# Optimization experiments

Hardware: AMD Instinct MI355X
Metric: run time of the kernel (lower is better)

Reference implementation:

```python
import jax, jax.numpy as jnp
import numpy as np

B, S, D, H = 2, 2048, 2048, 16
NOPE, ROPE, V, C = 128, 64, 128, 512
EPS = 1e-6


def _rope(x, cos, sin):
    # x: [b,s,h,d] with d even; consecutive pairs form complex numbers (torch view_as_complex)
    b, s, h, d = x.shape
    x2 = x.reshape(b, s, h, d // 2, 2)
    xr, xi = x2[..., 0], x2[..., 1]
    c = cos[None, :, None, :]
    sn = sin[None, :, None, :]
    yr = xr * c - xi * sn
    yi = xr * sn + xi * c
    return jnp.stack([yr, yi], axis=-1).reshape(b, s, h, d)


def _rmsnorm(x, w):
    return x * jax.lax.rsqrt(jnp.mean(x * x, axis=-1, keepdims=True) + EPS) * w


def setup_inputs() -> dict:
    key = jax.random.key(0)
    ks = jax.random.split(key, 6)
    x = jax.random.normal(ks[0], (B, S, D), jnp.float32)
    # xavier-ish scaled weights (torch layout: [out, in])
    wq = jax.random.normal(ks[1], (H * (NOPE + ROPE), D), jnp.float32) * (D ** -0.5)
    wkv_a = jax.random.normal(ks[2], (C + ROPE, D), jnp.float32) * (D ** -0.5)
    kv_norm_w = jnp.ones((C,), jnp.float32)
    wkv_b = jax.random.normal(ks[3], (H * (NOPE + V), C), jnp.float32) * (C ** -0.5)
    wo = jax.random.normal(ks[4], (D, H * V), jnp.float32) * ((H * V) ** -0.5)
    # rope freqs (theta=10000), cos/sin of shape [S, ROPE//2]
    inv = 1.0 / (10000.0 ** (np.arange(0, ROPE, 2, dtype=np.float32) / ROPE))
    ang = np.outer(np.arange(S, dtype=np.float32), inv)
    cos = jnp.asarray(np.cos(ang), jnp.float32)
    sin = jnp.asarray(np.sin(ang), jnp.float32)
    # causal additive mask [S, S]
    idx = jnp.arange(S)
    mask = jnp.where(idx[None, :] <= idx[:, None], 0.0, -1e9).astype(jnp.float32)
    return dict(x=x, cos=cos, sin=sin, mask=mask, wq=wq, wkv_a=wkv_a,
                kv_norm_w=kv_norm_w, wkv_b=wkv_b, wo=wo)


def reference(x, cos, sin, mask, wq, wkv_a, kv_norm_w, wkv_b, wo):
    scale = (NOPE + ROPE) ** -0.5
    # Q projection -> [B,S,H,NOPE+ROPE]
    q = (x @ wq.T).reshape(B, S, H, NOPE + ROPE)
    q_nope, q_pe = q[..., :NOPE], q[..., NOPE:]
    q_pe = _rope(q_pe, cos, sin)
    # low-rank KV latent + shared rope key
    kvr = x @ wkv_a.T                      # [B,S,C+ROPE]
    kv, k_pe = kvr[..., :C], kvr[..., C:]
    k_pe = _rope(k_pe[:, :, None, :], cos, sin)[:, :, 0, :]   # [B,S,ROPE]
    # absorb-mode: fold wkv_b's nope part into q
    wb = wkv_b.reshape(H, NOPE + V, C)
    q_abs = jnp.einsum('bshd,hdc->bshc', q_nope, wb[:, :NOPE])
    kvn = _rmsnorm(kv, kv_norm_w)          # latent cache [B,S,C]
    scores = (jnp.einsum('bshc,btc->bsht', q_abs, kvn)
              + jnp.einsum('bshr,btr->bsht', q_pe, k_pe)) * scale
    scores = scores + mask[None, :, None, :]
    p = jax.nn.softmax(scores.astype(jnp.float32), axis=-1).astype(x.dtype)
    o = jnp.einsum('bsht,btc->bshc', p, kvn)
    o = jnp.einsum('bshc,hdc->bshd', o, wb[:, NOPE:])   # un-absorb value proj
    return o.reshape(B, S, H * V) @ wo.T
```

## Files before the change

kernel.cpp:

```cpp
#include <hip/hip_runtime.h>
#include <hip/hip_bf16.h>

#define B_ 2
#define S_ 2048
#define H_ 16

typedef unsigned short ushort_t;
typedef unsigned int uint_t;
typedef __attribute__((ext_vector_type(8))) short bf16x8;
typedef __attribute__((ext_vector_type(4))) float f32x4;

__device__ __forceinline__ ushort_t f2bf(float f) {
    uint_t u = __float_as_uint(f);
    return (ushort_t)((u + 0x7fffu + ((u >> 16) & 1u)) >> 16);
}
__device__ __forceinline__ float bf2f(ushort_t v) {
    return __uint_as_float(((uint_t)v) << 16);
}

__device__ __forceinline__ void gl_lds16(const ushort_t* g, ushort_t* l) {
    __builtin_amdgcn_global_load_lds(
        (const __attribute__((address_space(1))) unsigned int*)(unsigned long long)g,
        (__attribute__((address_space(3))) unsigned int*)(unsigned int)(unsigned long long)l,
        16, 0, 0);
}

__global__ __launch_bounds__(256) void cast_bf16(const float* __restrict__ src,
                                                 ushort_t* __restrict__ dst, int n)
{
    int i = (blockIdx.x * 256 + threadIdx.x) * 4;
    if (i < n) {
        float4 v = *(const float4*)(src + i);
        ushort_t pk[4] = { f2bf(v.x), f2bf(v.y), f2bf(v.z), f2bf(v.w) };
        *(uint2*)(dst + i) = *(const uint2*)pk;
    }
}

__global__ __launch_bounds__(256) void cast2_bf16(const float* __restrict__ src,
                                                  ushort_t* __restrict__ hi,
                                                  ushort_t* __restrict__ lo, int n)
{
    int i = (blockIdx.x * 256 + threadIdx.x) * 4;
    if (i < n) {
        float4 v = *(const float4*)(src + i);
        float vv[4] = { v.x, v.y, v.z, v.w };
        ushort_t ph[4], pl[4];
#pragma unroll
        for (int k = 0; k < 4; k++) {
            ph[k] = f2bf(vv[k]);
            pl[k] = f2bf(vv[k] - bf2f(ph[k]));
        }
        *(uint2*)(hi + i) = *(const uint2*)ph;
        *(uint2*)(lo + i) = *(const uint2*)pl;
    }
}

__global__ __launch_bounds__(256, 2) void gemm_bf16(const ushort_t* __restrict__ A,
                                                    const ushort_t* __restrict__ Bm,
                                                    float* __restrict__ Cf,
                                                    ushort_t* __restrict__ Cb,
                                                    int M, int N, int K,
                                                    int ldc, int Nreal, int mode)
{
    __shared__ __align__(16) ushort_t As[2][8192];
    __shared__ __align__(16) ushort_t Bs[2][8192];
    const int tid = threadIdx.x;
    const int wv = tid >> 6, lane = tid & 63, l16 = lane & 15, quad = lane >> 4;
    const int wm = wv >> 1, wn = wv & 1;
    const int m0 = blockIdx.y * 128, n0 = blockIdx.x * 128;
    const int srow = lane >> 3;
    const int sch  = ((lane & 7) ^ srow) * 8;

    f32x4 acc[16];
#pragma unroll
    for (int i = 0; i < 16; i++) acc[i] = (f32x4)(0.f);

#pragma unroll
    for (int p = 0; p < 4; p++) {
        int g = wv + p*4, row = g*8 + srow;
        int rowb = n0 + row; if (rowb > Nreal - 1) rowb = Nreal - 1;
        gl_lds16(A  + (size_t)(m0 + row) * K + sch, &As[0][g*512]);
        gl_lds16(Bm + (size_t)rowb * K + sch,       &Bs[0][g*512]);
    }
    __syncthreads();

    int cur = 0;
    for (int k0 = 0; k0 < K; k0 += 64) {
        if (k0 + 64 < K) {
#pragma unroll
            for (int p = 0; p < 4; p++) {
                int g = wv + p*4, row = g*8 + srow;
                int rowb = n0 + row; if (rowb > Nreal - 1) rowb = Nreal - 1;
                gl_lds16(A  + (size_t)(m0 + row) * K + k0 + 64 + sch, &As[cur^1][g*512]);
                gl_lds16(Bm + (size_t)rowb * K + k0 + 64 + sch,       &Bs[cur^1][g*512]);
            }
        }
#pragma unroll
        for (int ks = 0; ks < 2; ks++) {
            bf16x8 af[4], bfr[4];
#pragma unroll
            for (int mt = 0; mt < 4; mt++) {
                int row = wm*64 + mt*16 + l16;
                af[mt] = *(const bf16x8*)(&As[cur][row*64 + (((ks*4+quad) ^ (l16&7))*8)]);
            }
#pragma unroll
            for (int nt = 0; nt < 4; nt++) {
                int row = wn*64 + nt*16 + l16;
                bfr[nt] = *(const bf16x8*)(&Bs[cur][row*64 + (((ks*4+quad) ^ (l16&7))*8)]);
            }
#pragma unroll
            for (int mt = 0; mt < 4; mt++)
#pragma unroll
                for (int nt = 0; nt < 4; nt++)
                    acc[mt*4+nt] = __builtin_amdgcn_mfma_f32_16x16x32_bf16(af[mt], bfr[nt], acc[mt*4+nt], 0, 0, 0);
        }
        __syncthreads();
        cur ^= 1;
    }
#pragma unroll
    for (int mt = 0; mt < 4; mt++)
#pragma unroll
        for (int nt = 0; nt < 4; nt++) {
            int cc = n0 + wn*64 + nt*16 + l16;
            if (cc < Nreal) {
#pragma unroll
                for (int r = 0; r < 4; r++) {
                    size_t rr = m0 + wm*64 + mt*16 + quad*4 + r;
                    float v = acc[mt*4+nt][r];
                    if (mode == 1)      Cb[rr*ldc + cc] = f2bf(v);
                    else if (mode == 2) Cf[rr*ldc + cc] += v;
                    else                Cf[rr*ldc + cc] = v;
                }
            }
        }
}

__global__ __launch_bounds__(256, 2) void gemm_kv3(const ushort_t* __restrict__ Ahg,
                                                   const ushort_t* __restrict__ Alg,
                                                   const ushort_t* __restrict__ Bhg,
                                                   const ushort_t* __restrict__ Blg,
                                                   float* __restrict__ Cf)
{
    __shared__ __align__(16) ushort_t Ah[8192];
    __shared__ __align__(16) ushort_t Al[8192];
    __shared__ __align__(16) ushort_t Bh[8192];
    __shared__ __align__(16) ushort_t Bl[8192];
    const int tid = threadIdx.x;
    const int wv = tid >> 6, lane = tid & 63, l16 = lane & 15, quad = lane >> 4;
    const int wm = wv >> 1, wn = wv & 1;
    const int m0 = blockIdx.y * 128, n0 = blockIdx.x * 128;
    const int srow = lane >> 3;
    const int sch  = ((lane & 7) ^ srow) * 8;
    const int K = 2048;

    f32x4 acc[16];
#pragma unroll
    for (int i = 0; i < 16; i++) acc[i] = (f32x4)(0.f);

    for (int k0 = 0; k0 < K; k0 += 64) {
#pragma unroll
        for (int p = 0; p < 4; p++) {
            int g = wv + p*4, row = g*8 + srow;
            int rowb = n0 + row; if (rowb > 575) rowb = 575;
            gl_lds16(Ahg + (size_t)(m0 + row)*K + k0 + sch, Ah + g*512);
            gl_lds16(Alg + (size_t)(m0 + row)*K + k0 + sch, Al + g*512);
            gl_lds16(Bhg + (size_t)rowb*K + k0 + sch,       Bh + g*512);
            gl_lds16(Blg + (size_t)rowb*K + k0 + sch,       Bl + g*512);
        }
        __syncthreads();
#pragma unroll
        for (int ks = 0; ks < 2; ks++) {
            bf16x8 ah[4], al[4], bh[4], bl[4];
#pragma unroll
            for (int mt = 0; mt < 4; mt++) {
                int off = (wm*64 + mt*16 + l16)*64 + (((ks*4+quad) ^ (l16&7))*8);
                ah[mt] = *(const bf16x8*)(Ah + off);
                al[mt] = *(const bf16x8*)(Al + off);
            }
#pragma unroll
            for (int nt = 0; nt < 4; nt++) {
                int off = (wn*64 + nt*16 + l16)*64 + (((ks*4+quad) ^ (l16&7))*8);
                bh[nt] = *(const bf16x8*)(Bh + off);
                bl[nt] = *(const bf16x8*)(Bl + off);
            }
#pragma unroll
            for (int mt = 0; mt < 4; mt++)
#pragma unroll
                for (int nt = 0; nt < 4; nt++) {
                    acc[mt*4+nt] = __builtin_amdgcn_mfma_f32_16x16x32_bf16(ah[mt], bh[nt], acc[mt*4+nt], 0, 0, 0);
                    acc[mt*4+nt] = __builtin_amdgcn_mfma_f32_16x16x32_bf16(al[mt], bh[nt], acc[mt*4+nt], 0, 0, 0);
                    acc[mt*4+nt] = __builtin_amdgcn_mfma_f32_16x16x32_bf16(ah[mt], bl[nt], acc[mt*4+nt], 0, 0, 0);
                }
        }
        __syncthreads();
    }
#pragma unroll
    for (int mt = 0; mt < 4; mt++)
#pragma unroll
        for (int nt = 0; nt < 4; nt++) {
            int cc = n0 + wn*64 + nt*16 + l16;
            if (cc < 576) {
#pragma unroll
                for (int r = 0; r < 4; r++) {
                    size_t rr = m0 + wm*64 + mt*16 + quad*4 + r;
                    Cf[rr*576 + cc] = acc[mt*4+nt][r];
                }
            }
        }
}

__global__ __launch_bounds__(256, 2) void gemm_vp(const ushort_t* __restrict__ kvnb,
                                                  const ushort_t* __restrict__ wbvB,
                                                  ushort_t* __restrict__ vpT)
{
    __shared__ __align__(16) ushort_t As[2][8192];
    __shared__ __align__(16) ushort_t Bs[2][8192];
    const int tid = threadIdx.x;
    const int wv = tid >> 6, lane = tid & 63, l16 = lane & 15, quad = lane >> 4;
    const int wm = wv >> 1, wn = wv & 1;
    const int m0 = blockIdx.x * 128;
    const int h  = blockIdx.y;
    const ushort_t* Bh = wbvB + h*65536;
    const int srow = lane >> 3;
    const int sch  = ((lane & 7) ^ srow) * 8;

    f32x4 acc[16];
#pragma unroll
    for (int i = 0; i < 16; i++) acc[i] = (f32x4)(0.f);

#pragma unroll
    for (int p = 0; p < 4; p++) {
        int g = wv + p*4, row = g*8 + srow;
        gl_lds16(kvnb + (size_t)(m0 + row)*512 + sch, &As[0][g*512]);
        gl_lds16(Bh   + (size_t)row*512 + sch,        &Bs[0][g*512]);
    }
    __syncthreads();

    int cur = 0;
    for (int k0 = 0; k0 < 512; k0 += 64) {
        if (k0 + 64 < 512) {
#pragma unroll
            for (int p = 0; p < 4; p++) {
                int g = wv + p*4, row = g*8 + srow;
                gl_lds16(kvnb + (size_t)(m0 + row)*512 + k0 + 64 + sch, &As[cur^1][g*512]);
                gl_lds16(Bh   + (size_t)row*512 + k0 + 64 + sch,        &Bs[cur^1][g*512]);
            }
        }
#pragma unroll
        for (int ks = 0; ks < 2; ks++) {
            bf16x8 af[4], bfr[4];
#pragma unroll
            for (int mt = 0; mt < 4; mt++) {
                int row = wm*64 + mt*16 + l16;
                af[mt] = *(const bf16x8*)(&As[cur][row*64 + (((ks*4+quad) ^ (l16&7))*8)]);
            }
#pragma unroll
            for (int nt = 0; nt < 4; nt++) {
                int row = wn*64 + nt*16 + l16;
                bfr[nt] = *(const bf16x8*)(&Bs[cur][row*64 + (((ks*4+quad) ^ (l16&7))*8)]);
            }
#pragma unroll
            for (int mt = 0; mt < 4; mt++)
#pragma unroll
                for (int nt = 0; nt < 4; nt++)
                    acc[mt*4+nt] = __builtin_amdgcn_mfma_f32_16x16x32_bf16(af[mt], bfr[nt], acc[mt*4+nt], 0, 0, 0);
        }
        __syncthreads();
        cur ^= 1;
    }
#pragma unroll
    for (int mt = 0; mt < 4; mt++)
#pragma unroll
        for (int nt = 0; nt < 4; nt++) {
            int rr = m0 + wm*64 + mt*16 + quad*4;
            int bb = rr >> 11, t = rr & 2047;
            int cc = wn*64 + nt*16 + l16;
            ushort_t pk[4];
#pragma unroll
            for (int r = 0; r < 4; r++) pk[r] = f2bf(acc[mt*4+nt][r]);
            *(uint2*)(vpT + ((size_t)((bb*16 + h)*128 + cc))*2048 + t) = *(const uint2*)pk;
        }
}

__global__ __launch_bounds__(256, 2) void gemm_kp(const ushort_t* __restrict__ kvnb,
                                                  const ushort_t* __restrict__ wbkN,
                                                  ushort_t* __restrict__ kpb)
{
    __shared__ __align__(16) ushort_t As[2][8192];
    __shared__ __align__(16) ushort_t Bs[2][8192];
    const int tid = threadIdx.x;
    const int wv = tid >> 6, lane = tid & 63, l16 = lane & 15, quad = lane >> 4;
    const int wm = wv >> 1, wn = wv & 1;
    const int m0 = blockIdx.x * 128;
    const int h  = blockIdx.y;
    const ushort_t* Bh = wbkN + h*65536;
    const int srow = lane >> 3;
    const int sch  = ((lane & 7) ^ srow) * 8;
    const float scale = 0.07216878364870323f;

    f32x4 acc[16];
#pragma unroll
    for (int i = 0; i < 16; i++) acc[i] = (f32x4)(0.f);

#pragma unroll
    for (int p = 0; p < 4; p++) {
        int g = wv + p*4, row = g*8 + srow;
        gl_lds16(kvnb + (size_t)(m0 + row)*512 + sch, &As[0][g*512]);
        gl_lds16(Bh   + (size_t)row*512 + sch,        &Bs[0][g*512]);
    }
    __syncthreads();

    int cur = 0;
    for (int k0 = 0; k0 < 512; k0 += 64) {
        if (k0 + 64 < 512) {
#pragma unroll
            for (int p = 0; p < 4; p++) {
                int g = wv + p*4, row = g*8 + srow;
                gl_lds16(kvnb + (size_t)(m0 + row)*512 + k0 + 64 + sch, &As[cur^1][g*512]);
                gl_lds16(Bh   + (size_t)row*512 + k0 + 64 + sch,        &Bs[cur^1][g*512]);
            }
        }
#pragma unroll
        for (int ks = 0; ks < 2; ks++) {
            bf16x8 af[4], bfr[4];
#pragma unroll
            for (int mt = 0; mt < 4; mt++) {
                int row = wm*64 + mt*16 + l16;
                af[mt] = *(const bf16x8*)(&As[cur][row*64 + (((ks*4+quad) ^ (l16&7))*8)]);
            }
#pragma unroll
            for (int nt = 0; nt < 4; nt++) {
                int row = wn*64 + nt*16 + l16;
                bfr[nt] = *(const bf16x8*)(&Bs[cur][row*64 + (((ks*4+quad) ^ (l16&7))*8)]);
            }
#pragma unroll
            for (int mt = 0; mt < 4; mt++)
#pragma unroll
                for (int nt = 0; nt < 4; nt++)
                    acc[mt*4+nt] = __builtin_amdgcn_mfma_f32_16x16x32_bf16(af[mt], bfr[nt], acc[mt*4+nt], 0, 0, 0);
        }
        __syncthreads();
        cur ^= 1;
    }
#pragma unroll
    for (int mt = 0; mt < 4; mt++)
#pragma unroll
        for (int nt = 0; nt < 4; nt++) {
            int cc = wn*64 + nt*16 + l16;
#pragma unroll
            for (int r = 0; r < 4; r++) {
                int rr = m0 + wm*64 + mt*16 + quad*4 + r;
                int bb = rr >> 11, t = rr & 2047;
                kpb[((size_t)((bb*16 + h)*2048 + t))*128 + cc] = f2bf(acc[mt*4+nt][r] * scale);
            }
        }
}

__global__ __launch_bounds__(256) void prep_wb(const float* __restrict__ wkv_b,
                                               ushort_t* __restrict__ wbkN,
                                               ushort_t* __restrict__ wbvB)
{
    int u = blockIdx.x * 256 + threadIdx.x;
    int h = u >> 16, rem = u & 65535;
    wbkN[u] = f2bf(wkv_b[h*131072 + rem]);
    wbvB[u] = f2bf(wkv_b[h*131072 + 65536 + rem]);
}

__global__ __launch_bounds__(256) void kv_norm_rope(const float* __restrict__ kvr,
                                                    const float* __restrict__ w,
                                                    const float* __restrict__ cosT,
                                                    const float* __restrict__ sinT,
                                                    ushort_t* __restrict__ kvnb,
                                                    ushort_t* __restrict__ kpeb)
{
    const int bs   = blockIdx.x * 4 + (threadIdx.x >> 6);
    const int lane = threadIdx.x & 63;
    const int s    = bs & (S_ - 1);
    const float* row = kvr + bs * 576;
    const float scale = 0.07216878364870323f;

    float4 v0 = *(const float4*)(row + lane*8);
    float4 v1 = *(const float4*)(row + lane*8 + 4);
    float ss = v0.x*v0.x + v0.y*v0.y + v0.z*v0.z + v0.w*v0.w
             + v1.x*v1.x + v1.y*v1.y + v1.z*v1.z + v1.w*v1.w;
#pragma unroll
    for (int off = 32; off >= 1; off >>= 1) ss += __shfl_xor(ss, off);
    const float rs = rsqrtf(ss * (1.0f/512.0f) + 1e-6f);

    float4 w0 = *(const float4*)(w + lane*8);
    float4 w1 = *(const float4*)(w + lane*8 + 4);
    float o[8];
    o[0] = v0.x*rs*w0.x; o[1] = v0.y*rs*w0.y; o[2] = v0.z*rs*w0.z; o[3] = v0.w*rs*w0.w;
    o[4] = v1.x*rs*w1.x; o[5] = v1.y*rs*w1.y; o[6] = v1.z*rs*w1.z; o[7] = v1.w*rs*w1.w;

    ushort_t pk[8];
#pragma unroll
    for (int p = 0; p < 8; p++) pk[p] = f2bf(o[p]);
    *(uint4*)(kvnb + (size_t)bs*512 + lane*8) = *(const uint4*)pk;

    if (lane < 32) {
        float xr = row[512 + 2*lane], xi = row[512 + 2*lane + 1];
        float c  = cosT[s*32 + lane], sn = sinT[s*32 + lane];
        ushort_t p2[2] = { f2bf((xr*c - xi*sn)*scale), f2bf((xr*sn + xi*c)*scale) };
        *(uint_t*)(kpeb + (size_t)bs*64 + 2*lane) = *(const uint_t*)p2;
    }
}

__device__ __forceinline__ void stage_tile(const ushort_t* kp_h, const ushort_t* kpe_b,
                                           const ushort_t* vpT_h, ushort_t* ldsb,
                                           int t0, int buf, int w, int l16, int q8e)
{
    ushort_t* Fb = ldsb + buf*6144;
    ushort_t* Vb = ldsb + 12288 + buf*4096;
#pragma unroll
    for (int ii = 0; ii < 3; ii++) {
        int i = w + ii*8;
        if (i < 12) {
            int g2 = (i >= 6) ? 1 : 0;
            int ks = i - g2*6;
            int row = t0 + g2*16 + l16;
            const ushort_t* src = (ks < 4)
                ? (kp_h + (size_t)row*128 + ks*32 + q8e)
                : (kpe_b + (size_t)row*64 + (ks-4)*32 + q8e);
            gl_lds16(src, Fb + i*512);
        } else if (i < 20) {
            int gv = i - 12;
            const ushort_t* src = vpT_h + (size_t)(gv*16 + l16)*2048 + t0 + q8e;
            gl_lds16(src, Vb + gv*512);
        }
    }
}

__global__ __launch_bounds__(512, 2) void attn_mfma(
    const ushort_t* __restrict__ qb,
    const ushort_t* __restrict__ kpb,
    const ushort_t* __restrict__ kpeb,
    const ushort_t* __restrict__ vpT,
    const float* __restrict__ cosT,
    const float* __restrict__ sinT,
    ushort_t* __restrict__ ovb)
{
    const int flat = blockIdx.x + 16*blockIdx.y + 256*blockIdx.z;
    const int b    = flat & 1;
    const int rem  = flat >> 1;
    const int h    = rem & 15;
    const int q0   = (15 - (rem >> 4)) << 7;

    const int tid  = threadIdx.x;
    const int w    = tid >> 6;
    const int lane = tid & 63;
    const int l16  = lane & 15;
    const int quad = lane >> 4;
    const int tl   = quad * 4;
    const int lb   = lane & 48;
    const int q8e  = quad * 8;

    __shared__ __align__(16) ushort_t lds[25600];

    const ushort_t* kp_h  = kpb + (size_t)(b*16 + h)*2048*128;
    const ushort_t* kpe_b = kpeb + (size_t)b*S_*64;
    const ushort_t* vpT_h = vpT + (size_t)(b*16 + h)*128*2048;

    const int r0    = q0 + w*16;
    const int rglob = r0 + l16;

    stage_tile(kp_h, kpe_b, vpT_h, lds, 0, 0, w, l16, q8e);

    const ushort_t* qrow = qb + (size_t)(b*S_ + rglob)*3072 + h*192;
    bf16x8 qf[6];
#pragma unroll
    for (int ks = 0; ks < 4; ks++)
        qf[ks] = *(const bf16x8*)(qrow + ks*32 + q8e);
#pragma unroll
    for (int kk = 0; kk < 2; kk++) {
        int off = kk*32 + q8e;
        uint4 pv4 = *(const uint4*)(qrow + 128 + off);
        const ushort_t* pe = (const ushort_t*)&pv4;
        ushort_t pk[8];
#pragma unroll
        for (int u2 = 0; u2 < 4; u2++) {
            float xr = bf2f(pe[2*u2]), xi = bf2f(pe[2*u2+1]);
            int pi = (off >> 1) + u2;
            float c = cosT[rglob*32 + pi], sn = sinT[rglob*32 + pi];
            pk[2*u2]   = f2bf(xr*c  - xi*sn);
            pk[2*u2+1] = f2bf(xr*sn + xi*c );
        }
        qf[4 + kk] = *(const bf16x8*)pk;
    }
    __syncthreads();

    f32x4 o[8];
#pragma unroll
    for (int n = 0; n < 8; n++) o[n] = (f32x4)(0.f);
    float m_s = -1e30f, l_s = 0.f;

    const int bniter = (q0 >> 5) + 4;
    const int wniter = ((r0 + 15) >> 5) + 1;
    ushort_t* ptw = lds + 20480 + w*640;
    int cur = 0;

#pragma unroll 1
    for (int it = 0; it < bniter; it++) {
        if (it + 1 < bniter)
            stage_tile(kp_h, kpe_b, vpT_h, lds, (it+1)*32, cur ^ 1, w, l16, q8e);

        if (it < wniter) {
            const int t0 = it * 32;
            const ushort_t* Fb = lds + cur*6144;
            const ushort_t* Vb = lds + 12288 + cur*4096;

            __builtin_amdgcn_s_setprio(1);
            f32x4 s0 = (f32x4)(0.f), s1 = (f32x4)(0.f);
#pragma unroll
            for (int ks = 0; ks < 6; ks++) {
                bf16x8 kf0 = *(const bf16x8*)(Fb + ks*512 + lane*8);
                s0 = __builtin_amdgcn_mfma_f32_16x16x32_bf16(kf0, qf[ks], s0, 0, 0, 0);
                bf16x8 kf1 = *(const bf16x8*)(Fb + 3072 + ks*512 + lane*8);
                s1 = __builtin_amdgcn_mfma_f32_16x16x32_bf16(kf1, qf[ks], s1, 0, 0, 0);
            }
            __builtin_amdgcn_s_setprio(0);

            float pv[8];
            float mx = -1e30f;
#pragma unroll
            for (int reg = 0; reg < 4; reg++) {
                pv[reg]   = ((t0 + tl + reg)      <= rglob) ? s0[reg] : -1e30f;
                pv[4+reg] = ((t0 + 16 + tl + reg) <= rglob) ? s1[reg] : -1e30f;
                mx = fmaxf(mx, fmaxf(pv[reg], pv[4+reg]));
            }
            mx = fmaxf(mx, __shfl_xor(mx, 16));
            mx = fmaxf(mx, __shfl_xor(mx, 32));
            if (!__all(mx <= m_s)) {
                float mn = fmaxf(m_s, mx);
                float al = __expf(m_s - mn);
                m_s = mn;
                l_s *= al;
                f32x4 alv;
#pragma unroll
                for (int reg = 0; reg < 4; reg++) alv[reg] = __shfl(al, lb + tl + reg, 64);
#pragma unroll
                for (int n = 0; n < 8; n++) o[n] *= alv;
            }
            float ps = 0.f;
#pragma unroll
            for (int reg = 0; reg < 8; reg++) {
                pv[reg] = (pv[reg] > -1e29f) ? __expf(pv[reg] - m_s) : 0.f;
                ps += pv[reg];
            }
            ps += __shfl_xor(ps, 16);
            ps += __shfl_xor(ps, 32);
            l_s += ps;

            ushort_t pk4[8];
#pragma unroll
            for (int reg = 0; reg < 8; reg++) pk4[reg] = f2bf(pv[reg]);
            *(uint2*)(ptw + l16*40 + tl)      = *(const uint2*)(pk4);
            *(uint2*)(ptw + l16*40 + 16 + tl) = *(const uint2*)(pk4 + 4);
            asm volatile("" ::: "memory");
            bf16x8 ap = *(const bf16x8*)(ptw + l16*40 + q8e);
            asm volatile("" ::: "memory");

            __builtin_amdgcn_s_setprio(1);
#pragma unroll
            for (int n = 0; n < 8; n++) {
                bf16x8 bv = *(const bf16x8*)(Vb + n*512 + lane*8);
                o[n] = __builtin_amdgcn_mfma_f32_16x16x32_bf16(ap, bv, o[n], 0, 0, 0);
            }
            __builtin_amdgcn_s_setprio(0);
        }
        __syncthreads();
        cur ^= 1;
    }

    float linv = 1.f / l_s;
    f32x4 rlv;
#pragma unroll
    for (int reg = 0; reg < 4; reg++) rlv[reg] = __shfl(linv, lb + tl + reg, 64);

    ushort_t* orow = ovb + (size_t)(b*S_ + r0)*2048 + h*128;
#pragma unroll
    for (int n = 0; n < 8; n++)
#pragma unroll
        for (int reg = 0; reg < 4; reg++)
            orow[(size_t)(tl + reg)*2048 + n*16 + l16] = f2bf(o[n][reg] * rlv[reg]);
}

extern "C" void kernel_launch(void* const* d_in, const int* in_sizes, int n_in,
                              void* d_out, int out_size, void* d_ws, size_t ws_size,
                              hipStream_t stream) {
    const float* x     = (const float*)d_in[0];
    const float* cosT  = (const float*)d_in[1];
    const float* sinT  = (const float*)d_in[2];
    const float* wq    = (const float*)d_in[4];
    const float* wkv_a = (const float*)d_in[5];
    const float* kvw   = (const float*)d_in[6];
    const float* wkv_b = (const float*)d_in[7];
    const float* wo    = (const float*)d_in[8];
    float* out = (float*)d_out;

    ushort_t* qb   = (ushort_t*)d_ws;
    ushort_t* xb   = qb   + 12582912;
    ushort_t* wqb  = xb   + 8388608;
    ushort_t* wob  = wqb  + 6291456;
    ushort_t* ovb  = wob  + 4194304;
    ushort_t* kvnb = ovb  + 8388608;
    ushort_t* kpeb = kvnb + 2097152;
    ushort_t* kvnT = kpeb + 262144;
    ushort_t* wbkN = kvnT + 2097152;
    ushort_t* wbvB = wbkN + 1048576;
    float*    kvr  = (float*)(wbvB + 1048576);

    ushort_t* xlo  = ovb;
    ushort_t* wahi = wqb;
    ushort_t* walo = wqb + 1179648;
    ushort_t* vpT  = xb;
    ushort_t* kpb  = wqb;

    dim3 blk(256);
    cast2_bf16<<<dim3(8192), blk, 0, stream>>>(x, xb, xlo, 8388608);
    cast_bf16<<<dim3(6144), blk, 0, stream>>>(wq, wqb, 6291456);
    prep_wb<<<dim3(4096), blk, 0, stream>>>(wkv_b, wbkN, wbvB);
    gemm_bf16<<<dim3(24, 32), blk, 0, stream>>>(xb, wqb, nullptr, qb, 4096, 3072, 2048, 3072, 3072, 1);
    cast2_bf16<<<dim3(1152), blk, 0, stream>>>(wkv_a, wahi, walo, 1179648);
    gemm_kv3<<<dim3(5, 32), blk, 0, stream>>>(xb, xlo, wahi, walo, kvr);
    kv_norm_rope<<<dim3(1024), blk, 0, stream>>>(kvr, kvw, cosT, sinT, kvnb, kpeb);
    gemm_vp<<<dim3(32, 16), blk, 0, stream>>>(kvnb, wbvB, vpT);
    gemm_kp<<<dim3(32, 16), blk, 0, stream>>>(kvnb, wbkN, kpb);
    attn_mfma<<<dim3(16, 16, 2), dim3(512), 0, stream>>>(qb, kpb, kpeb, vpT, cosT, sinT, ovb);
    cast_bf16<<<dim3(4096), blk, 0, stream>>>(wo, wob, 4194304);
    gemm_bf16<<<dim3(16, 32), blk, 0, stream>>>(ovb, wob, out, nullptr, 4096, 2048, 2048, 2048, 2048, 0);
}
```

Before: 478.9 us.

## Fuse K/V projection GEMMs, fold log2e into scale, skip masking on full tiles

Merges the separate key-projection and value-projection GEMMs into one kernel that loads the kvn tile once and accumulates against both weight halves. This removes a launch and a second read of kvn, but drops double-buffering and doubles accumulator registers. The attention scale now includes log2(e) so softmax can use exp2f. Causal masking is skipped for tiles lying fully below the diagonal, and probabilities are packed to bf16 with a hardware packed-convert instruction.

```diff
diff --git a/kernel.cpp b/kernel.cpp
--- a/kernel.cpp
+++ b/kernel.cpp
@@ -209,150 +209,75 @@
         }
 }
 
-__global__ __launch_bounds__(256, 2) void gemm_vp(const ushort_t* __restrict__ kvnb,
+__global__ __launch_bounds__(256, 2) void gemm_vk(const ushort_t* __restrict__ kvnb,
+                                                  const ushort_t* __restrict__ wbkN,
                                                   const ushort_t* __restrict__ wbvB,
+                                                  ushort_t* __restrict__ kpb,
                                                   ushort_t* __restrict__ vpT)
 {
-    __shared__ __align__(16) ushort_t As[2][8192];
-    __shared__ __align__(16) ushort_t Bs[2][8192];
+    __shared__ __align__(16) ushort_t As[8192];
+    __shared__ __align__(16) ushort_t Bk[8192];
+    __shared__ __align__(16) ushort_t Bv[8192];
     const int tid = threadIdx.x;
     const int wv = tid >> 6, lane = tid & 63, l16 = lane & 15, quad = lane >> 4;
     const int wm = wv >> 1, wn = wv & 1;
     const int m0 = blockIdx.x * 128;
     const int h  = blockIdx.y;
-    const ushort_t* Bh = wbvB + h*65536;
+    const ushort_t* Bkh = wbkN + h*65536;
+    const ushort_t* Bvh = wbvB + h*65536;
     const int srow = lane >> 3;
     const int sch  = ((lane & 7) ^ srow) * 8;
-
-    f32x4 acc[16];
-#pragma unroll
-    for (int i = 0; i < 16; i++) acc[i] = (f32x4)(0.f);
-
-#pragma unroll
-    for (int p = 0; p < 4; p++) {
-        int g = wv + p*4, row = g*8 + srow;
-        gl_lds16(kvnb + (size_t)(m0 + row)*512 + sch, &As[0][g*512]);
-        gl_lds16(Bh   + (size_t)row*512 + sch,        &Bs[0][g*512]);
-    }
-    __syncthreads();
-
-    int cur = 0;
+    const float SC2 = 0.10411756512f;
+
+    f32x4 ak[16], av[16];
+#pragma unroll
+    for (int i = 0; i < 16; i++) { ak[i] = (f32x4)(0.f); av[i] = (f32x4)(0.f); }
+
     for (int k0 = 0; k0 < 512; k0 += 64) {
-        if (k0 + 64 < 512) {
-#pragma unroll
-            for (int p = 0; p < 4; p++) {
-                int g = wv + p*4, row = g*8 + srow;
-                gl_lds16(kvnb + (size_t)(m0 + row)*512 + k0 + 64 + sch, &As[cur^1][g*512]);
-                gl_lds16(Bh   + (size_t)row*512 + k0 + 64 + sch,        &Bs[cur^1][g*512]);
-            }
-        }
+#pragma unroll
+        for (int p = 0; p < 4; p++) {
+            int g = wv + p*4, row = g*8 + srow;
+            gl_lds16(kvnb + (size_t)(m0 + row)*512 + k0 + sch, As + g*512);
+            gl_lds16(Bkh  + (size_t)row*512 + k0 + sch,        Bk + g*512);
+            gl_lds16(Bvh  + (size_t)row*512 + k0 + sch,        Bv + g*512);
+        }
+        __syncthreads();
 #pragma unroll
         for (int ks = 0; ks < 2; ks++) {
-            bf16x8 af[4], bfr[4];
-#pragma unroll
-            for (int mt = 0; mt < 4; mt++) {
-                int row = wm*64 + mt*16 + l16;
-                af[mt] = *(const bf16x8*)(&As[cur][row*64 + (((ks*4+quad) ^ (l16&7))*8)]);
-            }
+            bf16x8 af[4], bkf[4], bvf[4];
+#pragma unroll
+            for (int mt = 0; mt < 4; mt++)
+                af[mt] = *(const bf16x8*)(As + (wm*64 + mt*16 + l16)*64 + (((ks*4+quad) ^ (l16&7))*8));
 #pragma unroll
             for (int nt = 0; nt < 4; nt++) {
-                int row = wn*64 + nt*16 + l16;
-                bfr[nt] = *(const bf16x8*)(&Bs[cur][row*64 + (((ks*4+quad) ^ (l16&7))*8)]);
+                int off = (wn*64 + nt*16 + l16)*64 + (((ks*4+quad) ^ (l16&7))*8);
+                bkf[nt] = *(const bf16x8*)(Bk + off);
+                bvf[nt] = *(const bf16x8*)(Bv + off);
             }
 #pragma unroll
             for (int mt = 0; mt < 4; mt++)
 #pragma unroll
-                for (int nt = 0; nt < 4; nt++)
-                    acc[mt*4+nt] = __builtin_amdgcn_mfma_f32_16x16x32_bf16(af[mt], bfr[nt], acc[mt*4+nt], 0, 0, 0);
+                for (int nt = 0; nt < 4; nt++) {
+                    ak[mt*4+nt] = __builtin_amdgcn_mfma_f32_16x16x32_bf16(af[mt], bkf[nt], ak[mt*4+nt], 0, 0, 0);
+                    av[mt*4+nt] = __builtin_amdgcn_mfma_f32_16x16x32_bf16(af[mt], bvf[nt], av[mt*4+nt], 0, 0, 0);
+                }
         }
         __syncthreads();
-        cur ^= 1;
-    }
-#pragma unroll
-    for (int mt = 0; mt < 4; mt++)
-#pragma unroll
-        for (int nt = 0; nt < 4; nt++) {
-            int rr = m0 + wm*64 + mt*16 + quad*4;
-            int bb = rr >> 11, t = rr & 2047;
-            int cc = wn*64 + nt*16 + l16;
-            ushort_t pk[4];
-#pragma unroll
-            for (int r = 0; r < 4; r++) pk[r] = f2bf(acc[mt*4+nt][r]);
-            *(uint2*)(vpT + ((size_t)((bb*16 + h)*128 + cc))*2048 + t) = *(const uint2*)pk;
-        }
-}
-
-__global__ __launch_bounds__(256, 2) void gemm_kp(const ushort_t* __restrict__ kvnb,
-                                                  const ushort_t* __restrict__ wbkN,
-                                                  ushort_t* __restrict__ kpb)
-{
-    __shared__ __align__(16) ushort_t As[2][8192];
-    __shared__ __align__(16) ushort_t Bs[2][8192];
-    const int tid = threadIdx.x;
-    const int wv = tid >> 6, lane = tid & 63, l16 = lane & 15, quad = lane >> 4;
-    const int wm = wv >> 1, wn = wv & 1;
-    const int m0 = blockIdx.x * 128;
-    const int h  = blockIdx.y;
-    const ushort_t* Bh = wbkN + h*65536;
-    const int srow = lane >> 3;
-    const int sch  = ((lane & 7) ^ srow) * 8;
-    const float scale = 0.07216878364870323f;
-
-    f32x4 acc[16];
-#pragma unroll
-    for (int i = 0; i < 16; i++) acc[i] = (f32x4)(0.f);
-
-#pragma unroll
-    for (int p = 0; p < 4; p++) {
-        int g = wv + p*4, row = g*8 + srow;
-        gl_lds16(kvnb + (size_t)(m0 + row)*512 + sch, &As[0][g*512]);
-        gl_lds16(Bh   + (size_t)row*512 + sch,        &Bs[0][g*512]);
-    }
-    __syncthreads();
-
-    int cur = 0;
-    for (int k0 = 0; k0 < 512; k0 += 64) {
-        if (k0 + 64 < 512) {
-#pragma unroll
-            for (int p = 0; p < 4; p++) {
-                int g = wv + p*4, row = g*8 + srow;
-                gl_lds16(kvnb + (size_t)(m0 + row)*512 + k0 + 64 + sch, &As[cur^1][g*512]);
-                gl_lds16(Bh   + (size_t)row*512 + k0 + 64 + sch,        &Bs[cur^1][g*512]);
-            }
-        }
-#pragma unroll
-        for (int ks = 0; ks < 2; ks++) {
-            bf16x8 af[4], bfr[4];
-#pragma unroll
-            for (int mt = 0; mt < 4; mt++) {
-                int row = wm*64 + mt*16 + l16;
-                af[mt] = *(const bf16x8*)(&As[cur][row*64 + (((ks*4+quad) ^ (l16&7))*8)]);
-            }
-#pragma unroll
-            for (int nt = 0; nt < 4; nt++) {
-                int row = wn*64 + nt*16 + l16;
-                bfr[nt] = *(const bf16x8*)(&Bs[cur][row*64 + (((ks*4+quad) ^ (l16&7))*8)]);
-            }
-#pragma unroll
-            for (int mt = 0; mt < 4; mt++)
-#pragma unroll
-                for (int nt = 0; nt < 4; nt++)
-                    acc[mt*4+nt] = __builtin_amdgcn_mfma_f32_16x16x32_bf16(af[mt], bfr[nt], acc[mt*4+nt], 0, 0, 0);
-        }
-        __syncthreads();
-        cur ^= 1;
     }
 #pragma unroll
     for (int mt = 0; mt < 4; mt++)
 #pragma unroll
         for (int nt = 0; nt < 4; nt++) {
             int cc = wn*64 + nt*16 + l16;
-#pragma unroll
-            for (int r = 0; r < 4; r++) {
-                int rr = m0 + wm*64 + mt*16 + quad*4 + r;
-                int bb = rr >> 11, t = rr & 2047;
-                kpb[((size_t)((bb*16 + h)*2048 + t))*128 + cc] = f2bf(acc[mt*4+nt][r] * scale);
-            }
+            int rr0 = m0 + wm*64 + mt*16 + quad*4;
+            int bb = rr0 >> 11, t0 = rr0 & 2047;
+#pragma unroll
+            for (int r = 0; r < 4; r++)
+                kpb[((size_t)((bb*16 + h)*2048 + t0 + r))*128 + cc] = f2bf(ak[mt*4+nt][r] * SC2);
+            ushort_t pk[4];
+#pragma unroll
+            for (int r = 0; r < 4; r++) pk[r] = f2bf(av[mt*4+nt][r]);
+            *(uint2*)(vpT + ((size_t)((bb*16 + h)*128 + cc))*2048 + t0) = *(const uint2*)pk;
         }
 }
 
@@ -377,7 +302,7 @@
     const int lane = threadIdx.x & 63;
     const int s    = bs & (S_ - 1);
     const float* row = kvr + bs * 576;
-    const float scale = 0.07216878364870323f;
+    const float SC2 = 0.10411756512f;
 
     float4 v0 = *(const float4*)(row + lane*8);
     float4 v1 = *(const float4*)(row + lane*8 + 4);
@@ -401,7 +326,7 @@
     if (lane < 32) {
         float xr = row[512 + 2*lane], xi = row[512 + 2*lane + 1];
         float c  = cosT[s*32 + lane], sn = sinT[s*32 + lane];
-        ushort_t p2[2] = { f2bf((xr*c - xi*sn)*scale), f2bf((xr*sn + xi*c)*scale) };
+        ushort_t p2[2] = { f2bf((xr*c - xi*sn)*SC2), f2bf((xr*sn + xi*c)*SC2) };
         *(uint_t*)(kpeb + (size_t)bs*64 + 2*lane) = *(const uint_t*)p2;
     }
 }
@@ -521,18 +446,23 @@
             __builtin_amdgcn_s_setprio(0);
 
             float pv[8];
-            float mx = -1e30f;
-#pragma unroll
-            for (int reg = 0; reg < 4; reg++) {
-                pv[reg]   = ((t0 + tl + reg)      <= rglob) ? s0[reg] : -1e30f;
-                pv[4+reg] = ((t0 + 16 + tl + reg) <= rglob) ? s1[reg] : -1e30f;
-                mx = fmaxf(mx, fmaxf(pv[reg], pv[4+reg]));
-            }
+            if (t0 + 31 <= r0) {
+#pragma unroll
+                for (int reg = 0; reg < 4; reg++) { pv[reg] = s0[reg]; pv[4+reg] = s1[reg]; }
+            } else {
+#pragma unroll
+                for (int reg = 0; reg < 4; reg++) {
+                    pv[reg]   = ((t0 + tl + reg)      <= rglob) ? s0[reg] : -1e30f;
+                    pv[4+reg] = ((t0 + 16 + tl + reg) <= rglob) ? s1[reg] : -1e30f;
+                }
+            }
+            float mx = fmaxf(fmaxf(fmaxf(pv[0], pv[1]), fmaxf(pv[2], pv[3])),
+                             fmaxf(fmaxf(pv[4], pv[5]), fmaxf(pv[6], pv[7])));
             mx = fmaxf(mx, __shfl_xor(mx, 16));
             mx = fmaxf(mx, __shfl_xor(mx, 32));
             if (!__all(mx <= m_s)) {
                 float mn = fmaxf(m_s, mx);
-                float al = __expf(m_s - mn);
+                float al = exp2f(m_s - mn);
                 m_s = mn;
                 l_s *= al;
                 f32x4 alv;
@@ -544,18 +474,22 @@
             float ps = 0.f;
 #pragma unroll
             for (int reg = 0; reg < 8; reg++) {
-                pv[reg] = (pv[reg] > -1e29f) ? __expf(pv[reg] - m_s) : 0.f;
+                pv[reg] = exp2f(pv[reg] - m_s);
                 ps += pv[reg];
             }
             ps += __shfl_xor(ps, 16);
             ps += __shfl_xor(ps, 32);
             l_s += ps;
 
-            ushort_t pk4[8];
-#pragma unroll
-            for (int reg = 0; reg < 8; reg++) pk4[reg] = f2bf(pv[reg]);
-            *(uint2*)(ptw + l16*40 + tl)      = *(const uint2*)(pk4);
-            *(uint2*)(ptw + l16*40 + 16 + tl) = *(const uint2*)(pk4 + 4);
+            uint_t c01, c23, c45, c67;
+            asm("v_cvt_pk_bf16_f32 %0, %1, %2" : "=v"(c01) : "v"(pv[0]), "v"(pv[1]));
+            asm("v_cvt_pk_bf16_f32 %0, %1, %2" : "=v"(c23) : "v"(pv[2]), "v"(pv[3]));
+            asm("v_cvt_pk_bf16_f32 %0, %1, %2" : "=v"(c45) : "v"(pv[4]), "v"(pv[5]));
+            asm("v_cvt_pk_bf16_f32 %0, %1, %2" : "=v"(c67) : "v"(pv[6]), "v"(pv[7]));
+            uint2 plo; plo.x = c01; plo.y = c23;
+            uint2 phi; phi.x = c45; phi.y = c67;
+            *(uint2*)(ptw + l16*40 + tl)      = plo;
+            *(uint2*)(ptw + l16*40 + 16 + tl) = phi;
             asm volatile("" ::: "memory");
             bf16x8 ap = *(const bf16x8*)(ptw + l16*40 + q8e);
             asm volatile("" ::: "memory");
@@ -624,8 +558,7 @@
     cast2_bf16<<<dim3(1152), blk, 0, stream>>>(wkv_a, wahi, walo, 1179648);
     gemm_kv3<<<dim3(5, 32), blk, 0, stream>>>(xb, xlo, wahi, walo, kvr);
     kv_norm_rope<<<dim3(1024), blk, 0, stream>>>(kvr, kvw, cosT, sinT, kvnb, kpeb);
-    gemm_vp<<<dim3(32, 16), blk, 0, stream>>>(kvnb, wbvB, vpT);
-    gemm_kp<<<dim3(32, 16), blk, 0, stream>>>(kvnb, wbkN, kpb);
+    gemm_vk<<<dim3(32, 16), blk, 0, stream>>>(kvnb, wbkN, wbvB, kpb, vpT);
     attn_mfma<<<dim3(16, 16, 2), dim3(512), 0, stream>>>(qb, kpb, kpeb, vpT, cosT, sinT, ovb);
     cast_bf16<<<dim3(4096), blk, 0, stream>>>(wo, wob, 4194304);
     gemm_bf16<<<dim3(16, 32), blk, 0, stream>>>(ovb, wob, out, nullptr, 4096, 2048, 2048, 2048, 2048, 0);
```

After: 460.5 us. 3.8% less time.
